# Kernel tuning notes

Measured on AMD Instinct MI355X. Metric: run time of the kernel, lower is better.

## Reference

```python
import jax, jax.numpy as jnp
import numpy as np


def setup_inputs() -> dict:
    key = jax.random.key(0)
    kq, kv, kk = jax.random.split(key, 3)
    B, L, D = 16, 2048, 64
    q = jax.random.normal(kq, (B, L, D), dtype=jnp.float32)
    v = jax.random.normal(kv, (B, L, D), dtype=jnp.float32)
    k = jax.random.normal(kk, (B, L, D), dtype=jnp.float32)
    return {"q": q, "v": v, "k": k}


def reference(q, v, k):
    # scaled dot-product attention: bmm + softmax + (dropout=eval no-op) + bmm
    d = q.shape[-1]
    scores = jnp.einsum("bqd,bkd->bqk", q, k) / jnp.sqrt(jnp.asarray(d, q.dtype))
    attn = jax.nn.softmax(scores, axis=-1)  # torch F.softmax implicit dim resolves to last dim
    # dropout is identity in eval mode (deterministic reference)
    return jnp.einsum("bqk,bkd->bqd", attn, v)
```

## Files before the change

kernel.cpp:

```cpp
#include <hip/hip_runtime.h>


#define B_ 16
#define L_ 2048
#define D_ 64

typedef _Float16 f16;
typedef _Float16 f16x8 __attribute__((ext_vector_type(8)));
typedef _Float16 f16x4 __attribute__((ext_vector_type(4)));
typedef float f32x4 __attribute__((ext_vector_type(4)));

#define NKCHUNK (16 * 32 * 4 * 2)
#define NKTHREAD (NKCHUNK * 64)

__global__ __launch_bounds__(256) void pack_kv(const float* __restrict__ K,
                                               const float* __restrict__ V,
                                               f16* __restrict__ kf,
                                               f16* __restrict__ vf) {
  int id = blockIdx.x * 256 + threadIdx.x;
  if (id < NKTHREAD) {
    int l = id & 63, cid = id >> 6;
    int c = l & 15, g = l >> 4;
    int kc = cid & 1, mt = (cid >> 1) & 3, t = (cid >> 3) & 31, b = cid >> 8;
    const float* p = K + (size_t)(b * L_ + t * 64 + mt * 16 + c) * D_ + kc * 32 + g * 8;
    f32x4 x0 = *(const f32x4*)p;
    f32x4 x1 = *(const f32x4*)(p + 4);
    f16x8 o;
    o[0] = (f16)x0[0]; o[1] = (f16)x0[1]; o[2] = (f16)x0[2]; o[3] = (f16)x0[3];
    o[4] = (f16)x1[0]; o[5] = (f16)x1[1]; o[6] = (f16)x1[2]; o[7] = (f16)x1[3];
    *(f16x8*)(kf + (size_t)cid * 512 + l * 8) = o;
  } else {
    id -= NKTHREAD;
    int l = id & 63, cid = id >> 6;
    int c = l & 15, g = l >> 4;
    int h = cid & 1, dmt = (cid >> 1) & 3, t = (cid >> 3) & 31, b = cid >> 8;
    f16x8 o;
#pragma unroll
    for (int p2 = 0; p2 < 2; ++p2) {
#pragma unroll
      for (int j = 0; j < 4; ++j) {
        int kk = t * 64 + h * 32 + p2 * 16 + g * 4 + j;
        o[p2 * 4 + j] = (f16)V[(size_t)(b * L_ + kk) * D_ + dmt * 16 + c];
      }
    }
    *(f16x8*)(vf + (size_t)cid * 512 + l * 8) = o;
  }
}

__global__ __launch_bounds__(256, 4) void attn(const float* __restrict__ q,
                                               const f16* __restrict__ kf,
                                               const f16* __restrict__ vf,
                                               float* __restrict__ out) {
  int bid = blockIdx.x;
  int sub = bid >> 3;
  int b = (bid & 7) * 2 + (sub >> 6);
  int qb = sub & 63;
  int tid = threadIdx.x;
  int w = tid >> 6, l = tid & 63, c = l & 15, g = l >> 4;

  const float scale = 0.18033688011112042f;
  f16x8 qf[2][2];
#pragma unroll
  for (int nq = 0; nq < 2; ++nq) {
#pragma unroll
    for (int kc = 0; kc < 2; ++kc) {
      const float* p = q + (size_t)(b * L_ + qb * 32 + nq * 16 + c) * D_ + kc * 32 + g * 8;
      f32x4 x0 = *(const f32x4*)p, x1 = *(const f32x4*)(p + 4);
      f16x8 o;
      o[0] = (f16)(x0[0] * scale); o[1] = (f16)(x0[1] * scale);
      o[2] = (f16)(x0[2] * scale); o[3] = (f16)(x0[3] * scale);
      o[4] = (f16)(x1[0] * scale); o[5] = (f16)(x1[1] * scale);
      o[6] = (f16)(x1[2] * scale); o[7] = (f16)(x1[3] * scale);
      qf[nq][kc] = o;
    }
  }

  f32x4 O[4][2];
#pragma unroll
  for (int i = 0; i < 4; ++i)
#pragma unroll
    for (int j = 0; j < 2; ++j) O[i][j] = (f32x4){0.f, 0.f, 0.f, 0.f};
  f32x4 Zacc[2] = {(f32x4){0.f, 0.f, 0.f, 0.f}, (f32x4){0.f, 0.f, 0.f, 0.f}};
  const f16x4 ones = {(f16)1.f, (f16)1.f, (f16)1.f, (f16)1.f};
  const f32x4 Sinit = (f32x4){-8.f, -8.f, -8.f, -8.f};

  for (int t = w * 8; t < w * 8 + 8; ++t) {
    const f16* kbase = kf + (size_t)((b * 32 + t) * 8) * 512 + l * 8;
    f16x8 kfr[4][2];
#pragma unroll
    for (int mt = 0; mt < 4; ++mt)
#pragma unroll
      for (int kc = 0; kc < 2; ++kc)
        kfr[mt][kc] = *(const f16x8*)(kbase + (mt * 2 + kc) * 512);

    f32x4 S[4][2];
#pragma unroll
    for (int i = 0; i < 4; ++i)
#pragma unroll
      for (int j = 0; j < 2; ++j) S[i][j] = Sinit;
#pragma unroll
    for (int kc = 0; kc < 2; ++kc)
#pragma unroll
      for (int mt = 0; mt < 4; ++mt)
#pragma unroll
        for (int nq = 0; nq < 2; ++nq)
          S[mt][nq] = __builtin_amdgcn_mfma_f32_16x16x32_f16(kfr[mt][kc], qf[nq][kc],
                                                             S[mt][nq], 0, 0, 0);

    f16x4 pb[4][2];
#pragma unroll
    for (int nq = 0; nq < 2; ++nq)
#pragma unroll
      for (int mt = 0; mt < 4; ++mt) {
        f16x4 pv;
        pv[0] = (f16)__builtin_amdgcn_exp2f(S[mt][nq][0]);
        pv[1] = (f16)__builtin_amdgcn_exp2f(S[mt][nq][1]);
        pv[2] = (f16)__builtin_amdgcn_exp2f(S[mt][nq][2]);
        pv[3] = (f16)__builtin_amdgcn_exp2f(S[mt][nq][3]);
        pb[mt][nq] = pv;
      }

#pragma unroll
    for (int mt = 0; mt < 4; ++mt)
#pragma unroll
      for (int nq = 0; nq < 2; ++nq)
        Zacc[nq] = __builtin_amdgcn_mfma_f32_16x16x16f16(ones, pb[mt][nq], Zacc[nq], 0, 0, 0);

    const f16* vbase = vf + (size_t)((b * 32 + t) * 8) * 512 + l * 8;
#pragma unroll
    for (int dmt = 0; dmt < 4; ++dmt) {
#pragma unroll
      for (int h = 0; h < 2; ++h) {
        f16x8 vv = *(const f16x8*)(vbase + (dmt * 2 + h) * 512);
        f16x4 v0 = __builtin_shufflevector(vv, vv, 0, 1, 2, 3);
        f16x4 v1 = __builtin_shufflevector(vv, vv, 4, 5, 6, 7);
#pragma unroll
        for (int nq = 0; nq < 2; ++nq) {
          O[dmt][nq] = __builtin_amdgcn_mfma_f32_16x16x16f16(v0, pb[h * 2][nq], O[dmt][nq], 0, 0, 0);
          O[dmt][nq] = __builtin_amdgcn_mfma_f32_16x16x16f16(v1, pb[h * 2 + 1][nq], O[dmt][nq], 0, 0, 0);
        }
      }
    }
  }

  __shared__ float bufZ[4][2][16];
  __shared__ float bufO[2][64][36];

  if (l < 16) {
#pragma unroll
    for (int nq = 0; nq < 2; ++nq) bufZ[w][nq][l] = Zacc[nq][0];
  }
  if (w < 2) {
#pragma unroll
    for (int dmt = 0; dmt < 4; ++dmt)
#pragma unroll
      for (int nq = 0; nq < 2; ++nq)
#pragma unroll
        for (int r = 0; r < 4; ++r)
          bufO[w][dmt * 16 + g * 4 + r][nq * 16 + c] = O[dmt][nq][r];
  }
  __syncthreads();
  if (w >= 2) {
#pragma unroll
    for (int dmt = 0; dmt < 4; ++dmt)
#pragma unroll
      for (int nq = 0; nq < 2; ++nq)
#pragma unroll
        for (int r = 0; r < 4; ++r)
          bufO[w - 2][dmt * 16 + g * 4 + r][nq * 16 + c] += O[dmt][nq][r];
  }
  __syncthreads();

  int qq = tid >> 3, dc = tid & 7;
  int nqq = qq >> 4, cc = qq & 15;
  float Z = (bufZ[0][nqq][cc] + bufZ[1][nqq][cc]) + (bufZ[2][nqq][cc] + bufZ[3][nqq][cc]);
  float invZ = 1.0f / Z;
  float* op = out + (size_t)(b * L_ + qb * 32 + qq) * D_ + dc * 8;
#pragma unroll
  for (int u = 0; u < 2; ++u) {
    f32x4 acc;
#pragma unroll
    for (int i = 0; i < 4; ++i)
      acc[i] = (bufO[0][dc * 8 + u * 4 + i][qq] + bufO[1][dc * 8 + u * 4 + i][qq]) * invZ;
    *(f32x4*)(op + u * 4) = acc;
  }
}

extern "C" void kernel_launch(void* const* d_in, const int* in_sizes, int n_in,
                              void* d_out, int out_size, void* d_ws, size_t ws_size,
                              hipStream_t stream) {
  const float* q = (const float*)d_in[0];
  const float* v = (const float*)d_in[1];
  const float* k = (const float*)d_in[2];
  float* o = (float*)d_out;

  f16* kf = (f16*)d_ws;
  f16* vf = kf + (size_t)NKCHUNK * 512;

  pack_kv<<<(2 * NKTHREAD) / 256, 256, 0, stream>>>(k, v, kf, vf);
  attn<<<1024, 256, 0, stream>>>(q, kf, vf, o);
}
```

Measured before the change: 40.16 us.

## Double query tile to 64 rows per block with 8 waves splitting keys

Each block now handles 64 query rows instead of 32, and 8 waves each process 4 key tiles instead of 4 waves doing 8. Every K/V fragment loaded from global memory is reused across four query subtiles instead of two, so K/V traffic per query is halved. In exchange, per-wave register pressure roughly doubles for S, O and P, the final cross-wave reduction through shared memory takes more barrier steps, and the grid shrinks to 512 blocks.

```diff
diff --git a/kernel.cpp b/kernel.cpp
--- a/kernel.cpp
+++ b/kernel.cpp
@@ -47,24 +47,24 @@
   }
 }
 
-__global__ __launch_bounds__(256, 4) void attn(const float* __restrict__ q,
+__global__ __launch_bounds__(512, 4) void attn(const float* __restrict__ q,
                                                const f16* __restrict__ kf,
                                                const f16* __restrict__ vf,
                                                float* __restrict__ out) {
   int bid = blockIdx.x;
   int sub = bid >> 3;
-  int b = (bid & 7) * 2 + (sub >> 6);
-  int qb = sub & 63;
+  int b = (bid & 7) * 2 + (sub >> 5);
+  int qb = sub & 31;
   int tid = threadIdx.x;
   int w = tid >> 6, l = tid & 63, c = l & 15, g = l >> 4;
 
   const float scale = 0.18033688011112042f;
-  f16x8 qf[2][2];
-#pragma unroll
-  for (int nq = 0; nq < 2; ++nq) {
+  f16x8 qf[4][2];
+#pragma unroll
+  for (int nq = 0; nq < 4; ++nq) {
 #pragma unroll
     for (int kc = 0; kc < 2; ++kc) {
-      const float* p = q + (size_t)(b * L_ + qb * 32 + nq * 16 + c) * D_ + kc * 32 + g * 8;
+      const float* p = q + (size_t)(b * L_ + qb * 64 + nq * 16 + c) * D_ + kc * 32 + g * 8;
       f32x4 x0 = *(const f32x4*)p, x1 = *(const f32x4*)(p + 4);
       f16x8 o;
       o[0] = (f16)(x0[0] * scale); o[1] = (f16)(x0[1] * scale);
@@ -75,16 +75,18 @@
     }
   }
 
-  f32x4 O[4][2];
+  f32x4 O[4][4];
 #pragma unroll
   for (int i = 0; i < 4; ++i)
 #pragma unroll
-    for (int j = 0; j < 2; ++j) O[i][j] = (f32x4){0.f, 0.f, 0.f, 0.f};
-  f32x4 Zacc[2] = {(f32x4){0.f, 0.f, 0.f, 0.f}, (f32x4){0.f, 0.f, 0.f, 0.f}};
+    for (int j = 0; j < 4; ++j) O[i][j] = (f32x4){0.f, 0.f, 0.f, 0.f};
+  f32x4 Zacc[4];
+#pragma unroll
+  for (int j = 0; j < 4; ++j) Zacc[j] = (f32x4){0.f, 0.f, 0.f, 0.f};
   const f16x4 ones = {(f16)1.f, (f16)1.f, (f16)1.f, (f16)1.f};
   const f32x4 Sinit = (f32x4){-8.f, -8.f, -8.f, -8.f};
 
-  for (int t = w * 8; t < w * 8 + 8; ++t) {
+  for (int t = w * 4; t < w * 4 + 4; ++t) {
     const f16* kbase = kf + (size_t)((b * 32 + t) * 8) * 512 + l * 8;
     f16x8 kfr[4][2];
 #pragma unroll
@@ -93,23 +95,23 @@
       for (int kc = 0; kc < 2; ++kc)
         kfr[mt][kc] = *(const f16x8*)(kbase + (mt * 2 + kc) * 512);
 
-    f32x4 S[4][2];
+    f32x4 S[4][4];
 #pragma unroll
     for (int i = 0; i < 4; ++i)
 #pragma unroll
-      for (int j = 0; j < 2; ++j) S[i][j] = Sinit;
+      for (int j = 0; j < 4; ++j) S[i][j] = Sinit;
 #pragma unroll
     for (int kc = 0; kc < 2; ++kc)
 #pragma unroll
       for (int mt = 0; mt < 4; ++mt)
 #pragma unroll
-        for (int nq = 0; nq < 2; ++nq)
+        for (int nq = 0; nq < 4; ++nq)
           S[mt][nq] = __builtin_amdgcn_mfma_f32_16x16x32_f16(kfr[mt][kc], qf[nq][kc],
                                                              S[mt][nq], 0, 0, 0);
 
-    f16x4 pb[4][2];
-#pragma unroll
-    for (int nq = 0; nq < 2; ++nq)
+    f16x4 pb[4][4];
+#pragma unroll
+    for (int nq = 0; nq < 4; ++nq)
 #pragma unroll
       for (int mt = 0; mt < 4; ++mt) {
         f16x4 pv;
@@ -123,7 +125,7 @@
 #pragma unroll
     for (int mt = 0; mt < 4; ++mt)
 #pragma unroll
-      for (int nq = 0; nq < 2; ++nq)
+      for (int nq = 0; nq < 4; ++nq)
         Zacc[nq] = __builtin_amdgcn_mfma_f32_16x16x16f16(ones, pb[mt][nq], Zacc[nq], 0, 0, 0);
 
     const f16* vbase = vf + (size_t)((b * 32 + t) * 8) * 512 + l * 8;
@@ -135,7 +137,7 @@
         f16x4 v0 = __builtin_shufflevector(vv, vv, 0, 1, 2, 3);
         f16x4 v1 = __builtin_shufflevector(vv, vv, 4, 5, 6, 7);
 #pragma unroll
-        for (int nq = 0; nq < 2; ++nq) {
+        for (int nq = 0; nq < 4; ++nq) {
           O[dmt][nq] = __builtin_amdgcn_mfma_f32_16x16x16f16(v0, pb[h * 2][nq], O[dmt][nq], 0, 0, 0);
           O[dmt][nq] = __builtin_amdgcn_mfma_f32_16x16x16f16(v1, pb[h * 2 + 1][nq], O[dmt][nq], 0, 0, 0);
         }
@@ -143,39 +145,59 @@
     }
   }
 
-  __shared__ float bufZ[4][2][16];
-  __shared__ float bufO[2][64][36];
+  __shared__ float bufZ[8][68];
+  __shared__ float bufO[2][64][68];
 
   if (l < 16) {
 #pragma unroll
-    for (int nq = 0; nq < 2; ++nq) bufZ[w][nq][l] = Zacc[nq][0];
+    for (int nq = 0; nq < 4; ++nq) bufZ[w][nq * 16 + l] = Zacc[nq][0];
   }
   if (w < 2) {
 #pragma unroll
     for (int dmt = 0; dmt < 4; ++dmt)
 #pragma unroll
-      for (int nq = 0; nq < 2; ++nq)
+      for (int nq = 0; nq < 4; ++nq)
 #pragma unroll
         for (int r = 0; r < 4; ++r)
           bufO[w][dmt * 16 + g * 4 + r][nq * 16 + c] = O[dmt][nq][r];
   }
   __syncthreads();
-  if (w >= 2) {
-#pragma unroll
-    for (int dmt = 0; dmt < 4; ++dmt)
-#pragma unroll
-      for (int nq = 0; nq < 2; ++nq)
+  if (w == 2 || w == 3) {
+#pragma unroll
+    for (int dmt = 0; dmt < 4; ++dmt)
+#pragma unroll
+      for (int nq = 0; nq < 4; ++nq)
 #pragma unroll
         for (int r = 0; r < 4; ++r)
           bufO[w - 2][dmt * 16 + g * 4 + r][nq * 16 + c] += O[dmt][nq][r];
   }
   __syncthreads();
+  if (w == 4 || w == 5) {
+#pragma unroll
+    for (int dmt = 0; dmt < 4; ++dmt)
+#pragma unroll
+      for (int nq = 0; nq < 4; ++nq)
+#pragma unroll
+        for (int r = 0; r < 4; ++r)
+          bufO[w - 4][dmt * 16 + g * 4 + r][nq * 16 + c] += O[dmt][nq][r];
+  }
+  __syncthreads();
+  if (w >= 6) {
+#pragma unroll
+    for (int dmt = 0; dmt < 4; ++dmt)
+#pragma unroll
+      for (int nq = 0; nq < 4; ++nq)
+#pragma unroll
+        for (int r = 0; r < 4; ++r)
+          bufO[w - 6][dmt * 16 + g * 4 + r][nq * 16 + c] += O[dmt][nq][r];
+  }
+  __syncthreads();
 
   int qq = tid >> 3, dc = tid & 7;
-  int nqq = qq >> 4, cc = qq & 15;
-  float Z = (bufZ[0][nqq][cc] + bufZ[1][nqq][cc]) + (bufZ[2][nqq][cc] + bufZ[3][nqq][cc]);
+  float Z = ((bufZ[0][qq] + bufZ[1][qq]) + (bufZ[2][qq] + bufZ[3][qq])) +
+            ((bufZ[4][qq] + bufZ[5][qq]) + (bufZ[6][qq] + bufZ[7][qq]));
   float invZ = 1.0f / Z;
-  float* op = out + (size_t)(b * L_ + qb * 32 + qq) * D_ + dc * 8;
+  float* op = out + (size_t)(b * L_ + qb * 64 + qq) * D_ + dc * 8;
 #pragma unroll
   for (int u = 0; u < 2; ++u) {
     f32x4 acc;
@@ -198,5 +220,5 @@
   f16* vf = kf + (size_t)NKCHUNK * 512;
 
   pack_kv<<<(2 * NKTHREAD) / 256, 256, 0, stream>>>(k, v, kf, vf);
-  attn<<<1024, 256, 0, stream>>>(q, kf, vf, o);
+  attn<<<512, 512, 0, stream>>>(q, kf, vf, o);
 }
```

Measured after the change: 125.6 us. 213% more time.
